# Optimization experiments

Hardware: AMD Instinct MI355X
Metric: run time of the kernel (lower is better)

The kernel has to match this reference:

```python
import jax, jax.numpy as jnp
import numpy as np

N, L, S, C, H = 8, 1024, 1024, 512, 8
SCALE = float((C // H) ** 0.5)  # sqrt(64), as in source (based on embed_dim, not cat'd dim)


def _linear_params(key, c_in, c_out):
    kw, kb = jax.random.split(key)
    lim = 1.0 / np.sqrt(c_in)
    W = jax.random.uniform(kw, (c_out, c_in), jnp.float32, -lim, lim)
    b = jax.random.uniform(kb, (c_out,), jnp.float32, -lim, lim)
    return W, b


def setup_inputs() -> dict:
    key = jax.random.key(0)
    ks = jax.random.split(key, 12)
    inp = {
        'q_c': jax.random.normal(ks[0], (N, L, C), jnp.float32),
        'q_p': jax.random.normal(ks[1], (N, L, C), jnp.float32),
        'k_c': jax.random.normal(ks[2], (N, S, C), jnp.float32),
        'k_p': jax.random.normal(ks[3], (N, S, C), jnp.float32),
        'v': jax.random.normal(ks[4], (N, S, C), jnp.float32),
        'attn_mask': jax.random.normal(ks[5], (N, H, L, S), jnp.float32),
    }
    for i, name in enumerate(['qc', 'qp', 'kc', 'kp', 'v', 'o']):
        W, b = _linear_params(ks[6 + i], C, C)
        inp[f'W_{name}'] = W
        inp[f'b_{name}'] = b
    return inp


def _split_head(x, h):
    n, l, c = x.shape
    return x.reshape(n, l, h, c // h).transpose(0, 2, 1, 3)  # (N,H,L,c/h)


def reference(q_c, q_p, k_c, k_p, v, attn_mask,
              W_qc, b_qc, W_qp, b_qp, W_kc, b_kc, W_kp, b_kp, W_v, b_v, W_o, b_o):
    # dual projections + cat -> (N, L, 2C)
    q = jnp.concatenate([q_c @ W_qc.T + b_qc, q_p @ W_qp.T + b_qp], axis=-1)
    k = jnp.concatenate([k_c @ W_kc.T + b_kc, k_p @ W_kp.T + b_kp], axis=-1)
    vv = v @ W_v.T + b_v
    q = _split_head(q, H)   # (N,H,L,2C/H)
    k = _split_head(k, H)   # (N,H,S,2C/H)
    vv = _split_head(vv, H)  # (N,H,S,C/H)
    attn = jnp.einsum('nhld,nhsd->nhls', q / SCALE, k) + attn_mask
    attn = jax.nn.softmax(attn, axis=-1)
    out = jnp.einsum('nhls,nhsd->nhld', attn, vv)
    out = out.transpose(0, 2, 1, 3).reshape(N, L, C)
    return out @ W_o.T + b_o
```

## Files before the change

### kernel.cpp

```cpp
#include <hip/hip_runtime.h>
#include <hip/hip_bf16.h>

typedef __bf16 bf16;
typedef __bf16 bf16x8 __attribute__((ext_vector_type(8)));
typedef float  f32x4  __attribute__((ext_vector_type(4)));
typedef float  f32x2  __attribute__((ext_vector_type(2)));

#define LOG2E        1.4426950408889634f
#define QSCALE_LOG2E 0.18033688011112043f
#define DEFER_THR    20.0f

#define GLDS(g, l)                                                        \
  __builtin_amdgcn_global_load_lds(                                       \
      (const __attribute__((address_space(1))) void*)(g),                 \
      (__attribute__((address_space(3))) void*)(l), 16, 0, 0)

#define WAITV(n) asm volatile("s_waitcnt vmcnt(" #n ")" ::: "memory")
#define BARRIER() do {                                                    \
  __builtin_amdgcn_s_barrier();                                           \
  __builtin_amdgcn_sched_barrier(0);                                      \
} while (0)

__device__ __forceinline__ void stage_f32_tile(const float* __restrict__ src, int ld,
                                               char* dst, int tid) {
  #pragma unroll
  for (int t = 0; t < 8; ++t) {
    int c8  = tid + t * 256;
    int row = c8 >> 4;
    int h8  = c8 & 15;
    const f32x4 v = *reinterpret_cast<const f32x4*>(src + row * ld + h8 * 4);
    union { bf16 h[4]; unsigned long long u; } pk;
    pk.h[0] = (bf16)v[0]; pk.h[1] = (bf16)v[1];
    pk.h[2] = (bf16)v[2]; pk.h[3] = (bf16)v[3];
    int byte = (row << 7) + ((((h8 >> 1) ^ (row & 7)) << 4) | ((h8 & 1) << 3));
    *reinterpret_cast<unsigned long long*>(dst + byte) = pk.u;
  }
}

__device__ __forceinline__ void stage_bf16_tile(const bf16* __restrict__ src, int ld,
                                                char* dst, int tid) {
  #pragma unroll
  for (int t = 0; t < 4; ++t) {
    int c   = tid + t * 256;
    int row = c >> 3;
    int ck  = c & 7;
    const bf16x8 v = *reinterpret_cast<const bf16x8*>(src + row * ld + ck * 8);
    int byte = (row << 7) + (((ck ^ (row & 7)) << 4));
    *reinterpret_cast<bf16x8*>(dst + byte) = v;
  }
}

__global__ __launch_bounds__(256) void proj_gemm(
    const float* __restrict__ qc, const float* __restrict__ qp,
    const float* __restrict__ kc, const float* __restrict__ kp,
    const float* __restrict__ vin,
    const float* __restrict__ Wqc, const float* __restrict__ bqc,
    const float* __restrict__ Wqp, const float* __restrict__ bqp,
    const float* __restrict__ Wkc, const float* __restrict__ bkc,
    const float* __restrict__ Wkp, const float* __restrict__ bkp,
    const float* __restrict__ Wv,  const float* __restrict__ bv,
    bf16* __restrict__ Qws, bf16* __restrict__ Kws, bf16* __restrict__ Vtws) {
  __shared__ __align__(16) bf16 lA[128 * 64];
  __shared__ __align__(16) bf16 lB[128 * 64];
  char* lAb = (char*)lA;
  char* lBb = (char*)lB;

  const int bxr = blockIdx.x;
  const int bx  = (bxr & 7) * 160 + (bxr >> 3);
  const int g  = bx >> 8;
  const int mt = (bx & 255) >> 2;
  const int nt = bx & 3;

  const float *A, *W, *bias;
  if      (g == 0) { A = qc;  W = Wqc; bias = bqc; }
  else if (g == 1) { A = qp;  W = Wqp; bias = bqp; }
  else if (g == 2) { A = kc;  W = Wkc; bias = bkc; }
  else if (g == 3) { A = kp;  W = Wkp; bias = bkp; }
  else             { A = vin; W = Wv;  bias = bv;  }

  const int tid  = threadIdx.x;
  const int lane = tid & 63, wid = tid >> 6;
  const int wr = wid >> 1, wc = wid & 1;
  const int lrow = lane & 15, lgrp = lane >> 4;

  const float* Abase = A + (size_t)(mt * 128) * 512;
  const float* Wbase = W + (size_t)(nt * 128) * 512;

  const f32x4 fz = {0.f, 0.f, 0.f, 0.f};
  f32x4 acc[4][4];
  #pragma unroll
  for (int i = 0; i < 4; ++i)
    #pragma unroll
    for (int j = 0; j < 4; ++j) acc[i][j] = fz;

  for (int k0 = 0; k0 < 512; k0 += 64) {
    __syncthreads();
    stage_f32_tile(Abase + k0, 512, lAb, tid);
    stage_f32_tile(Wbase + k0, 512, lBb, tid);
    __syncthreads();
    #pragma unroll
    for (int kk = 0; kk < 2; ++kk) {
      bf16x8 af[4], bfr[4];
      #pragma unroll
      for (int mf = 0; mf < 4; ++mf) {
        int row  = wr * 64 + mf * 16 + lrow;
        int byte = (row << 7) + ((((kk << 2) | lgrp) ^ (row & 7)) << 4);
        af[mf] = *reinterpret_cast<const bf16x8*>(lAb + byte);
      }
      #pragma unroll
      for (int nf = 0; nf < 4; ++nf) {
        int row  = wc * 64 + nf * 16 + lrow;
        int byte = (row << 7) + ((((kk << 2) | lgrp) ^ (row & 7)) << 4);
        bfr[nf] = *reinterpret_cast<const bf16x8*>(lBb + byte);
      }
      #pragma unroll
      for (int mf = 0; mf < 4; ++mf)
        #pragma unroll
        for (int nf = 0; nf < 4; ++nf)
          acc[mf][nf] = __builtin_amdgcn_mfma_f32_16x16x32_bf16(
              af[mf], bfr[nf], acc[mf][nf], 0, 0, 0);
    }
  }

  float bcol[4];
  #pragma unroll
  for (int nf = 0; nf < 4; ++nf)
    bcol[nf] = bias[nt * 128 + wc * 64 + nf * 16 + lrow];

  #pragma unroll
  for (int mf = 0; mf < 4; ++mf) {
    #pragma unroll
    for (int nf = 0; nf < 4; ++nf) {
      #pragma unroll
      for (int r = 0; r < 4; ++r) {
        int grow = mt * 128 + wr * 64 + mf * 16 + lgrp * 4 + r;
        int col  = nt * 128 + wc * 64 + nf * 16 + lrow;
        float vv = acc[mf][nf][r] + bcol[nf];
        bf16 hb  = (bf16)vv;
        int n = grow >> 10, tt = grow & 1023;
        if (g < 2) {
          int j = (g << 9) + col;
          Qws[(size_t)((((n << 3) + (j >> 7)) << 10) | tt) * 128 + (j & 127)] = hb;
        } else if (g < 4) {
          int j  = ((g - 2) << 9) + col;
          int hh = j >> 7, d = j & 127;
          int dd = (((d >> 3) ^ ((tt >> 1) & 7)) << 3) | (d & 7);
          Kws[(size_t)((((n << 3) + hh) << 10) | tt) * 128 + dd] = hb;
        } else {
          int h = col >> 6, d = col & 63;
          int kt2 = tt >> 5, si = tt & 31;
          int ss = (((si >> 3) ^ ((d >> 1) & 3)) << 3) | (si & 7);
          Vtws[((size_t)((((n << 3) + h) << 5) + kt2) * 64 + d) * 32 + ss] = hb;
        }
      }
    }
  }
}

__global__ __launch_bounds__(256) void attn_fwd(
    const bf16* __restrict__ Qws, const bf16* __restrict__ Kws,
    const bf16* __restrict__ Vtws, const float* __restrict__ mask,
    bf16* __restrict__ Ows) {
  __shared__ __align__(16) char Kl[3][8192];
  __shared__ __align__(16) char Vl[3][4096];
  __shared__ __align__(16) char Ml[5][8192];
  __shared__ __align__(16) char Pl[4][1024];

  const int bxr = blockIdx.x;
  const int bx  = (bxr & 7) * 128 + (bxr >> 3);
  const int nh = bx >> 4;
  const int qt = bx & 15;
  const int tid = threadIdx.x;
  const int lane = tid & 63, wid = tid >> 6;
  const int lrow = lane & 15, lgrp = lane >> 4;
  const int q0 = qt * 64 + wid * 16;

  const bf16* Qb = Qws + ((size_t)(nh * 1024 + q0 + lrow)) * 128 + lgrp * 8;
  bf16x8 qf[4];
  #pragma unroll
  for (int kk = 0; kk < 4; ++kk)
    qf[kk] = *reinterpret_cast<const bf16x8*>(Qb + kk * 32);

  const float* Mg = mask + ((size_t)(nh * 1024) + qt * 64 + (lane >> 3)) * 1024 +
                    (lane & 7) * 4;
  const bf16* Kg = Kws + (size_t)nh * 131072 + lane * 8;
  const bf16* Vg = Vtws + (size_t)nh * 65536 + lane * 8;

  char* Pb = &Pl[wid][0];

  const f32x4 fz = {0.f, 0.f, 0.f, 0.f};
  f32x4 oacc[4];
  #pragma unroll
  for (int dt = 0; dt < 4; ++dt) oacc[dt] = fz;
  float m2[4], lsum[4];
  #pragma unroll
  for (int r = 0; r < 4; ++r) { m2[r] = 0.f; lsum[r] = 0.f; }

  auto stageM = [&](char* dst, int kt) {
    if (wid == 0) {
      #pragma unroll
      for (int i = 0; i < 8; ++i)
        GLDS(Mg + i * 8192 + kt * 32, dst + i * 1024);
    }
  };
  auto stageKV = [&](char* Kd, char* Vd, int kt) {
    if (wid == 1 || wid == 2) {
      #pragma unroll
      for (int j = 0; j < 4; ++j)
        GLDS(Kg + kt * 4096 + (wid - 1) * 2048 + j * 512,
             Kd + (wid - 1) * 4096 + j * 1024);
    } else if (wid == 3) {
      #pragma unroll
      for (int j = 0; j < 4; ++j)
        GLDS(Vg + kt * 2048 + j * 512, Vd + j * 1024);
    }
  };

  auto compute = [&](const char* Kb, const char* Vb, const char* Mb) {
    bf16x8 kf0[4], kf1[4], vf[4];
    #pragma unroll
    for (int kk = 0; kk < 4; ++kk) {
      int cb = ((((kk << 2) | lgrp) ^ (lrow & 7)) << 4);
      kf0[kk] = *reinterpret_cast<const bf16x8*>(Kb + lrow * 512 + cb);
      kf1[kk] = *reinterpret_cast<const bf16x8*>(Kb + lrow * 512 + 256 + cb);
    }
    #pragma unroll
    for (int dt = 0; dt < 4; ++dt)
      vf[dt] = *reinterpret_cast<const bf16x8*>(
          Vb + (dt * 16 + lrow) * 64 + ((lgrp ^ ((lrow >> 1) & 3)) << 4));
    f32x2 mk[4];
    #pragma unroll
    for (int r = 0; r < 4; ++r) {
      int qrow = wid * 16 + lgrp * 4 + r;
      mk[r] = *reinterpret_cast<const f32x2*>(Mb + qrow * 128 + lrow * 8);
    }

    f32x4 sc0 = fz, sc1 = fz;
    __builtin_amdgcn_s_setprio(1);
    #pragma unroll
    for (int kk = 0; kk < 4; ++kk)
      sc0 = __builtin_amdgcn_mfma_f32_16x16x32_bf16(qf[kk], kf0[kk], sc0, 0, 0, 0);
    #pragma unroll
    for (int kk = 0; kk < 4; ++kk)
      sc1 = __builtin_amdgcn_mfma_f32_16x16x32_bf16(qf[kk], kf1[kk], sc1, 0, 0, 0);
    __builtin_amdgcn_s_setprio(0);

    float a0r[4], a1r[4];
    bool ok = true;
    #pragma unroll
    for (int r = 0; r < 4; ++r) {
      a0r[r] = fmaf(sc0[r], QSCALE_LOG2E, mk[r].x * LOG2E);
      a1r[r] = fmaf(sc1[r], QSCALE_LOG2E, mk[r].y * LOG2E);
      ok &= (fmaxf(a0r[r], a1r[r]) <= m2[r] + DEFER_THR);
    }
    if (__builtin_expect(!__all(ok), 0)) {
      #pragma unroll
      for (int r = 0; r < 4; ++r) {
        float tv = fmaxf(a0r[r], a1r[r]);
        tv = fmaxf(tv, __shfl_xor(tv, 1));
        tv = fmaxf(tv, __shfl_xor(tv, 2));
        tv = fmaxf(tv, __shfl_xor(tv, 4));
        tv = fmaxf(tv, __shfl_xor(tv, 8));
        float mn = fmaxf(m2[r], tv);
        float corr = exp2f(m2[r] - mn);
        m2[r] = mn;
        lsum[r] *= corr;
        #pragma unroll
        for (int dt = 0; dt < 4; ++dt) oacc[dt][r] *= corr;
      }
    }
    #pragma unroll
    for (int r = 0; r < 4; ++r) {
      float e0 = exp2f(a0r[r] - m2[r]);
      float e1 = exp2f(a1r[r] - m2[r]);
      lsum[r] += e0 + e1;
      union { bf16 h[2]; unsigned u; } pk;
      pk.h[0] = (bf16)e0; pk.h[1] = (bf16)e1;
      int row = lgrp * 4 + r;
      int byte = row * 64 + ((((lrow >> 2) ^ (row & 3)) << 4) | ((lrow & 3) << 2));
      *reinterpret_cast<unsigned*>(Pb + byte) = pk.u;
    }
    __builtin_amdgcn_wave_barrier();
    __builtin_amdgcn_sched_barrier(0);
    bf16x8 pf = *reinterpret_cast<const bf16x8*>(
        Pb + lrow * 64 + ((lgrp ^ (lrow & 3)) << 4));

    __builtin_amdgcn_s_setprio(1);
    #pragma unroll
    for (int dt = 0; dt < 4; ++dt)
      oacc[dt] = __builtin_amdgcn_mfma_f32_16x16x32_bf16(pf, vf[dt], oacc[dt], 0, 0, 0);
    __builtin_amdgcn_s_setprio(0);
  };

  char *ka = &Kl[0][0], *kb2 = &Kl[1][0], *kc2 = &Kl[2][0];
  char *va = &Vl[0][0], *vb2 = &Vl[1][0], *vc2 = &Vl[2][0];
  char *m0 = &Ml[0][0], *m1 = &Ml[1][0], *m2p = &Ml[2][0],
       *m3 = &Ml[3][0], *m4 = &Ml[4][0];
  auto rotKV = [&]() {
    char* tp = ka; ka = kb2; kb2 = kc2; kc2 = tp;
    tp = va; va = vb2; vb2 = vc2; vc2 = tp;
  };
  auto rotM = [&]() {
    char* tp = m0; m0 = m1; m1 = m2p; m2p = m3; m3 = m4; m4 = tp;
  };

  stageKV(ka, va, 0);
  stageKV(kb2, vb2, 1);
  stageM(m0, 0); stageM(m1, 1); stageM(m2p, 2); stageM(m3, 3);
  if (wid == 0) { WAITV(24); } else { WAITV(4); }
  BARRIER();

  for (int t = 0; t < 28; ++t) {
    stageKV(kc2, vc2, t + 2);
    stageM(m4, t + 4);
    compute(ka, va, m0);
    if (wid == 0) { WAITV(24); } else { WAITV(4); }
    BARRIER();
    rotKV(); rotM();
  }
  stageKV(kc2, vc2, 30);
  compute(ka, va, m0);
  if (wid == 0) { WAITV(16); } else { WAITV(4); }
  BARRIER(); rotKV(); rotM();

  stageKV(kc2, vc2, 31);
  compute(ka, va, m0);
  if (wid == 0) { WAITV(8); } else { WAITV(4); }
  BARRIER(); rotKV(); rotM();

  compute(ka, va, m0);
  WAITV(0);
  BARRIER(); rotKV(); rotM();

  compute(ka, va, m0);

  #pragma unroll
  for (int r = 0; r < 4; ++r) {
    float ss = lsum[r];
    ss += __shfl_xor(ss, 1);
    ss += __shfl_xor(ss, 2);
    ss += __shfl_xor(ss, 4);
    ss += __shfl_xor(ss, 8);
    lsum[r] = 1.0f / ss;
  }

  const int n = nh >> 3, h = nh & 7;
  bf16* Ob = Ows + ((size_t)(n * 1024 + q0 + lgrp * 4)) * 512 + h * 64 + lrow;
  #pragma unroll
  for (int dt = 0; dt < 4; ++dt)
    #pragma unroll
    for (int r = 0; r < 4; ++r)
      Ob[(size_t)r * 512 + dt * 16] = (bf16)(oacc[dt][r] * lsum[r]);
}

__global__ __launch_bounds__(256) void out_gemm(
    const bf16* __restrict__ Ows, const float* __restrict__ Wo,
    const float* __restrict__ bo, float* __restrict__ out) {
  __shared__ __align__(16) bf16 lA[128 * 64];
  __shared__ __align__(16) bf16 lB[128 * 64];
  char* lAb = (char*)lA;
  char* lBb = (char*)lB;

  const int bxr = blockIdx.x;
  const int bx  = (bxr & 7) * 32 + (bxr >> 3);
  const int mt = bx >> 2;
  const int nt = bx & 3;
  const int tid = threadIdx.x;
  const int lane = tid & 63, wid = tid >> 6;
  const int wr = wid >> 1, wc = wid & 1;
  const int lrow = lane & 15, lgrp = lane >> 4;

  const bf16*  Abase = Ows + (size_t)(mt * 128) * 512;
  const float* Wbase = Wo  + (size_t)(nt * 128) * 512;

  const f32x4 fz = {0.f, 0.f, 0.f, 0.f};
  f32x4 acc[4][4];
  #pragma unroll
  for (int i = 0; i < 4; ++i)
    #pragma unroll
    for (int j = 0; j < 4; ++j) acc[i][j] = fz;

  for (int k0 = 0; k0 < 512; k0 += 64) {
    __syncthreads();
    stage_bf16_tile(Abase + k0, 512, lAb, tid);
    stage_f32_tile(Wbase + k0, 512, lBb, tid);
    __syncthreads();
    #pragma unroll
    for (int kk = 0; kk < 2; ++kk) {
      bf16x8 af[4], bfr[4];
      #pragma unroll
      for (int mf = 0; mf < 4; ++mf) {
        int row  = wr * 64 + mf * 16 + lrow;
        int byte = (row << 7) + ((((kk << 2) | lgrp) ^ (row & 7)) << 4);
        af[mf] = *reinterpret_cast<const bf16x8*>(lAb + byte);
      }
      #pragma unroll
      for (int nf = 0; nf < 4; ++nf) {
        int row  = wc * 64 + nf * 16 + lrow;
        int byte = (row << 7) + ((((kk << 2) | lgrp) ^ (row & 7)) << 4);
        bfr[nf] = *reinterpret_cast<const bf16x8*>(lBb + byte);
      }
      #pragma unroll
      for (int mf = 0; mf < 4; ++mf)
        #pragma unroll
        for (int nf = 0; nf < 4; ++nf)
          acc[mf][nf] = __builtin_amdgcn_mfma_f32_16x16x32_bf16(
              af[mf], bfr[nf], acc[mf][nf], 0, 0, 0);
    }
  }

  float bcol[4];
  #pragma unroll
  for (int nf = 0; nf < 4; ++nf)
    bcol[nf] = bo[nt * 128 + wc * 64 + nf * 16 + lrow];

  #pragma unroll
  for (int mf = 0; mf < 4; ++mf) {
    #pragma unroll
    for (int nf = 0; nf < 4; ++nf) {
      #pragma unroll
      for (int r = 0; r < 4; ++r) {
        int grow = mt * 128 + wr * 64 + mf * 16 + lgrp * 4 + r;
        int col  = nt * 128 + wc * 64 + nf * 16 + lrow;
        out[(size_t)grow * 512 + col] = acc[mf][nf][r] + bcol[nf];
      }
    }
  }
}

extern "C" void kernel_launch(void* const* d_in, const int* in_sizes, int n_in,
                              void* d_out, int out_size, void* d_ws, size_t ws_size,
                              hipStream_t stream) {
  const float* qc   = (const float*)d_in[0];
  const float* qp   = (const float*)d_in[1];
  const float* kc   = (const float*)d_in[2];
  const float* kp   = (const float*)d_in[3];
  const float* vin  = (const float*)d_in[4];
  const float* mask = (const float*)d_in[5];
  const float* Wqc  = (const float*)d_in[6];
  const float* bqc  = (const float*)d_in[7];
  const float* Wqp  = (const float*)d_in[8];
  const float* bqp  = (const float*)d_in[9];
  const float* Wkc  = (const float*)d_in[10];
  const float* bkc  = (const float*)d_in[11];
  const float* Wkp  = (const float*)d_in[12];
  const float* bkp  = (const float*)d_in[13];
  const float* Wv   = (const float*)d_in[14];
  const float* bv   = (const float*)d_in[15];
  const float* Wo   = (const float*)d_in[16];
  const float* bo   = (const float*)d_in[17];

  bf16* Qws  = (bf16*)d_ws;
  bf16* Kws  = Qws  + (size_t)8 * 1024 * 1024;
  bf16* Vtws = Kws  + (size_t)8 * 1024 * 1024;
  bf16* Ows  = Vtws + (size_t)4 * 1024 * 1024;

  proj_gemm<<<dim3(1280), dim3(256), 0, stream>>>(
      qc, qp, kc, kp, vin, Wqc, bqc, Wqp, bqp, Wkc, bkc, Wkp, bkp, Wv, bv,
      Qws, Kws, Vtws);
  attn_fwd<<<dim3(1024), dim3(256), 0, stream>>>(Qws, Kws, Vtws, mask, Ows);
  out_gemm<<<dim3(256), dim3(256), 0, stream>>>(Ows, Wo, bo, (float*)d_out);
}
```

Before: 183.9 us.

## Double KV tile width per iteration and shallow the prefetch pipeline

```diff
diff --git a/kernel.cpp b/kernel.cpp
--- a/kernel.cpp
+++ b/kernel.cpp
@@ -161,10 +161,10 @@
     const bf16* __restrict__ Qws, const bf16* __restrict__ Kws,
     const bf16* __restrict__ Vtws, const float* __restrict__ mask,
     bf16* __restrict__ Ows) {
-  __shared__ __align__(16) char Kl[3][8192];
-  __shared__ __align__(16) char Vl[3][4096];
-  __shared__ __align__(16) char Ml[5][8192];
-  __shared__ __align__(16) char Pl[4][1024];
+  __shared__ __align__(16) char Kl[2][16384];
+  __shared__ __align__(16) char Vl[2][8192];
+  __shared__ __align__(16) char Ml[3][16384];
+  __shared__ __align__(16) char Pl[4][2][1024];
 
   const int bxr = blockIdx.x;
   const int bx  = (bxr & 7) * 128 + (bxr >> 3);
@@ -181,12 +181,13 @@
   for (int kk = 0; kk < 4; ++kk)
     qf[kk] = *reinterpret_cast<const bf16x8*>(Qb + kk * 32);
 
-  const float* Mg = mask + ((size_t)(nh * 1024) + qt * 64 + (lane >> 3)) * 1024 +
-                    (lane & 7) * 4;
+  const float* Mg = mask + ((size_t)(nh * 1024) + qt * 64 + (lane >> 4)) * 1024 +
+                    (lane & 15) * 4;
   const bf16* Kg = Kws + (size_t)nh * 131072 + lane * 8;
   const bf16* Vg = Vtws + (size_t)nh * 65536 + lane * 8;
 
-  char* Pb = &Pl[wid][0];
+  char* PbA = &Pl[wid][0][0];
+  char* PbB = &Pl[wid][1][0];
 
   const f32x4 fz = {0.f, 0.f, 0.f, 0.f};
   f32x4 oacc[4];
@@ -199,64 +200,73 @@
   auto stageM = [&](char* dst, int kt) {
     if (wid == 0) {
       #pragma unroll
-      for (int i = 0; i < 8; ++i)
-        GLDS(Mg + i * 8192 + kt * 32, dst + i * 1024);
+      for (int i = 0; i < 16; ++i)
+        GLDS(Mg + (size_t)i * 4096 + kt * 64, dst + i * 1024);
     }
   };
   auto stageKV = [&](char* Kd, char* Vd, int kt) {
     if (wid == 1 || wid == 2) {
       #pragma unroll
-      for (int j = 0; j < 4; ++j)
-        GLDS(Kg + kt * 4096 + (wid - 1) * 2048 + j * 512,
-             Kd + (wid - 1) * 4096 + j * 1024);
+      for (int j = 0; j < 8; ++j)
+        GLDS(Kg + kt * 8192 + (wid - 1) * 4096 + j * 512,
+             Kd + (wid - 1) * 8192 + j * 1024);
     } else if (wid == 3) {
       #pragma unroll
-      for (int j = 0; j < 4; ++j)
-        GLDS(Vg + kt * 2048 + j * 512, Vd + j * 1024);
+      for (int j = 0; j < 8; ++j)
+        GLDS(Vg + kt * 4096 + j * 512, Vd + j * 1024);
     }
   };
 
   auto compute = [&](const char* Kb, const char* Vb, const char* Mb) {
-    bf16x8 kf0[4], kf1[4], vf[4];
+    bf16x8 ka0[4], ka1[4], kb0[4], kb1[4], vfA[4], vfB[4];
     #pragma unroll
     for (int kk = 0; kk < 4; ++kk) {
       int cb = ((((kk << 2) | lgrp) ^ (lrow & 7)) << 4);
-      kf0[kk] = *reinterpret_cast<const bf16x8*>(Kb + lrow * 512 + cb);
-      kf1[kk] = *reinterpret_cast<const bf16x8*>(Kb + lrow * 512 + 256 + cb);
-    }
-    #pragma unroll
-    for (int dt = 0; dt < 4; ++dt)
-      vf[dt] = *reinterpret_cast<const bf16x8*>(
-          Vb + (dt * 16 + lrow) * 64 + ((lgrp ^ ((lrow >> 1) & 3)) << 4));
-    f32x2 mk[4];
+      ka0[kk] = *reinterpret_cast<const bf16x8*>(Kb + lrow * 512 + cb);
+      ka1[kk] = *reinterpret_cast<const bf16x8*>(Kb + lrow * 512 + 256 + cb);
+      kb0[kk] = *reinterpret_cast<const bf16x8*>(Kb + 8192 + lrow * 512 + cb);
+      kb1[kk] = *reinterpret_cast<const bf16x8*>(Kb + 8192 + lrow * 512 + 256 + cb);
+    }
+    #pragma unroll
+    for (int dt = 0; dt < 4; ++dt) {
+      int vb = (dt * 16 + lrow) * 64 + ((lgrp ^ ((lrow >> 1) & 3)) << 4);
+      vfA[dt] = *reinterpret_cast<const bf16x8*>(Vb + vb);
+      vfB[dt] = *reinterpret_cast<const bf16x8*>(Vb + 4096 + vb);
+    }
+    f32x2 mkA[4], mkB[4];
     #pragma unroll
     for (int r = 0; r < 4; ++r) {
       int qrow = wid * 16 + lgrp * 4 + r;
-      mk[r] = *reinterpret_cast<const f32x2*>(Mb + qrow * 128 + lrow * 8);
-    }
-
-    f32x4 sc0 = fz, sc1 = fz;
+      mkA[r] = *reinterpret_cast<const f32x2*>(Mb + qrow * 256 + lrow * 8);
+      mkB[r] = *reinterpret_cast<const f32x2*>(Mb + qrow * 256 + 128 + lrow * 8);
+    }
+
+    f32x4 sA0 = fz, sA1 = fz, sB0 = fz, sB1 = fz;
     __builtin_amdgcn_s_setprio(1);
     #pragma unroll
-    for (int kk = 0; kk < 4; ++kk)
-      sc0 = __builtin_amdgcn_mfma_f32_16x16x32_bf16(qf[kk], kf0[kk], sc0, 0, 0, 0);
-    #pragma unroll
-    for (int kk = 0; kk < 4; ++kk)
-      sc1 = __builtin_amdgcn_mfma_f32_16x16x32_bf16(qf[kk], kf1[kk], sc1, 0, 0, 0);
+    for (int kk = 0; kk < 4; ++kk) {
+      sA0 = __builtin_amdgcn_mfma_f32_16x16x32_bf16(qf[kk], ka0[kk], sA0, 0, 0, 0);
+      sA1 = __builtin_amdgcn_mfma_f32_16x16x32_bf16(qf[kk], ka1[kk], sA1, 0, 0, 0);
+      sB0 = __builtin_amdgcn_mfma_f32_16x16x32_bf16(qf[kk], kb0[kk], sB0, 0, 0, 0);
+      sB1 = __builtin_amdgcn_mfma_f32_16x16x32_bf16(qf[kk], kb1[kk], sB1, 0, 0, 0);
+    }
     __builtin_amdgcn_s_setprio(0);
 
-    float a0r[4], a1r[4];
+    float aA0[4], aA1[4], aB0[4], aB1[4];
     bool ok = true;
     #pragma unroll
     for (int r = 0; r < 4; ++r) {
-      a0r[r] = fmaf(sc0[r], QSCALE_LOG2E, mk[r].x * LOG2E);
-      a1r[r] = fmaf(sc1[r], QSCALE_LOG2E, mk[r].y * LOG2E);
-      ok &= (fmaxf(a0r[r], a1r[r]) <= m2[r] + DEFER_THR);
+      aA0[r] = fmaf(sA0[r], QSCALE_LOG2E, mkA[r].x * LOG2E);
+      aA1[r] = fmaf(sA1[r], QSCALE_LOG2E, mkA[r].y * LOG2E);
+      aB0[r] = fmaf(sB0[r], QSCALE_LOG2E, mkB[r].x * LOG2E);
+      aB1[r] = fmaf(sB1[r], QSCALE_LOG2E, mkB[r].y * LOG2E);
+      float mx = fmaxf(fmaxf(aA0[r], aA1[r]), fmaxf(aB0[r], aB1[r]));
+      ok &= (mx <= m2[r] + DEFER_THR);
     }
     if (__builtin_expect(!__all(ok), 0)) {
       #pragma unroll
       for (int r = 0; r < 4; ++r) {
-        float tv = fmaxf(a0r[r], a1r[r]);
+        float tv = fmaxf(fmaxf(aA0[r], aA1[r]), fmaxf(aB0[r], aB1[r]));
         tv = fmaxf(tv, __shfl_xor(tv, 1));
         tv = fmaxf(tv, __shfl_xor(tv, 2));
         tv = fmaxf(tv, __shfl_xor(tv, 4));
@@ -271,68 +281,67 @@
     }
     #pragma unroll
     for (int r = 0; r < 4; ++r) {
-      float e0 = exp2f(a0r[r] - m2[r]);
-      float e1 = exp2f(a1r[r] - m2[r]);
-      lsum[r] += e0 + e1;
-      union { bf16 h[2]; unsigned u; } pk;
-      pk.h[0] = (bf16)e0; pk.h[1] = (bf16)e1;
+      float eA0 = exp2f(aA0[r] - m2[r]);
+      float eA1 = exp2f(aA1[r] - m2[r]);
+      float eB0 = exp2f(aB0[r] - m2[r]);
+      float eB1 = exp2f(aB1[r] - m2[r]);
+      lsum[r] += (eA0 + eA1) + (eB0 + eB1);
       int row = lgrp * 4 + r;
       int byte = row * 64 + ((((lrow >> 2) ^ (row & 3)) << 4) | ((lrow & 3) << 2));
-      *reinterpret_cast<unsigned*>(Pb + byte) = pk.u;
+      union { bf16 h[2]; unsigned u; } pa, pb;
+      pa.h[0] = (bf16)eA0; pa.h[1] = (bf16)eA1;
+      pb.h[0] = (bf16)eB0; pb.h[1] = (bf16)eB1;
+      *reinterpret_cast<unsigned*>(PbA + byte) = pa.u;
+      *reinterpret_cast<unsigned*>(PbB + byte) = pb.u;
     }
     __builtin_amdgcn_wave_barrier();
     __builtin_amdgcn_sched_barrier(0);
-    bf16x8 pf = *reinterpret_cast<const bf16x8*>(
-        Pb + lrow * 64 + ((lgrp ^ (lrow & 3)) << 4));
+    int pby = lrow * 64 + ((lgrp ^ (lrow & 3)) << 4);
+    bf16x8 pfA = *reinterpret_cast<const bf16x8*>(PbA + pby);
+    bf16x8 pfB = *reinterpret_cast<const bf16x8*>(PbB + pby);
 
     __builtin_amdgcn_s_setprio(1);
     #pragma unroll
     for (int dt = 0; dt < 4; ++dt)
-      oacc[dt] = __builtin_amdgcn_mfma_f32_16x16x32_bf16(pf, vf[dt], oacc[dt], 0, 0, 0);
+      oacc[dt] = __builtin_amdgcn_mfma_f32_16x16x32_bf16(pfA, vfA[dt], oacc[dt], 0, 0, 0);
+    #pragma unroll
+    for (int dt = 0; dt < 4; ++dt)
+      oacc[dt] = __builtin_amdgcn_mfma_f32_16x16x32_bf16(pfB, vfB[dt], oacc[dt], 0, 0, 0);
     __builtin_amdgcn_s_setprio(0);
   };
 
-  char *ka = &Kl[0][0], *kb2 = &Kl[1][0], *kc2 = &Kl[2][0];
-  char *va = &Vl[0][0], *vb2 = &Vl[1][0], *vc2 = &Vl[2][0];
-  char *m0 = &Ml[0][0], *m1 = &Ml[1][0], *m2p = &Ml[2][0],
-       *m3 = &Ml[3][0], *m4 = &Ml[4][0];
-  auto rotKV = [&]() {
-    char* tp = ka; ka = kb2; kb2 = kc2; kc2 = tp;
-    tp = va; va = vb2; vb2 = vc2; vc2 = tp;
-  };
-  auto rotM = [&]() {
-    char* tp = m0; m0 = m1; m1 = m2p; m2p = m3; m3 = m4; m4 = tp;
-  };
-
-  stageKV(ka, va, 0);
-  stageKV(kb2, vb2, 1);
-  stageM(m0, 0); stageM(m1, 1); stageM(m2p, 2); stageM(m3, 3);
-  if (wid == 0) { WAITV(24); } else { WAITV(4); }
+  char *kcur = &Kl[0][0], *knxt = &Kl[1][0];
+  char *vcur = &Vl[0][0], *vnxt = &Vl[1][0];
+  char *m0 = &Ml[0][0], *m1 = &Ml[1][0], *m2p = &Ml[2][0];
+
+  stageKV(kcur, vcur, 0);
+  stageM(m0, 0);
+  stageM(m1, 1);
+  if (wid == 0) { WAITV(16); } else { WAITV(0); }
   BARRIER();
 
-  for (int t = 0; t < 28; ++t) {
-    stageKV(kc2, vc2, t + 2);
-    stageM(m4, t + 4);
-    compute(ka, va, m0);
-    if (wid == 0) { WAITV(24); } else { WAITV(4); }
+  for (int t = 0; t < 14; ++t) {
+    stageKV(knxt, vnxt, t + 1);
+    stageM(m2p, t + 2);
+    compute(kcur, vcur, m0);
+    if (wid == 0) { WAITV(16); } else { WAITV(0); }
     BARRIER();
-    rotKV(); rotM();
-  }
-  stageKV(kc2, vc2, 30);
-  compute(ka, va, m0);
-  if (wid == 0) { WAITV(16); } else { WAITV(4); }
-  BARRIER(); rotKV(); rotM();
-
-  stageKV(kc2, vc2, 31);
-  compute(ka, va, m0);
-  if (wid == 0) { WAITV(8); } else { WAITV(4); }
-  BARRIER(); rotKV(); rotM();
-
-  compute(ka, va, m0);
+    char* tp;
+    tp = kcur; kcur = knxt; knxt = tp;
+    tp = vcur; vcur = vnxt; vnxt = tp;
+    tp = m0; m0 = m1; m1 = m2p; m2p = tp;
+  }
+  stageKV(knxt, vnxt, 15);
+  compute(kcur, vcur, m0);
   WAITV(0);
-  BARRIER(); rotKV(); rotM();
-
-  compute(ka, va, m0);
+  BARRIER();
+  {
+    char* tp;
+    tp = kcur; kcur = knxt; knxt = tp;
+    tp = vcur; vcur = vnxt; vnxt = tp;
+    tp = m0; m0 = m1; m1 = m2p; m2p = tp;
+  }
+  compute(kcur, vcur, m0);
 
   #pragma unroll
   for (int r = 0; r < 4; ++r) {
```

New measurement: 200.3 us. 8.9% more time.

## Pre-convert projection weights to bf16 and restructure proj GEMM tiling

Applied to the files above, without the earlier changes.

```diff
diff --git a/kernel.cpp b/kernel.cpp
--- a/kernel.cpp
+++ b/kernel.cpp
@@ -21,120 +21,147 @@
   __builtin_amdgcn_sched_barrier(0);                                      \
 } while (0)
 
-__device__ __forceinline__ void stage_f32_tile(const float* __restrict__ src, int ld,
-                                               char* dst, int tid) {
-  #pragma unroll
-  for (int t = 0; t < 8; ++t) {
-    int c8  = tid + t * 256;
-    int row = c8 >> 4;
-    int h8  = c8 & 15;
-    const f32x4 v = *reinterpret_cast<const f32x4*>(src + row * ld + h8 * 4);
-    union { bf16 h[4]; unsigned long long u; } pk;
-    pk.h[0] = (bf16)v[0]; pk.h[1] = (bf16)v[1];
-    pk.h[2] = (bf16)v[2]; pk.h[3] = (bf16)v[3];
-    int byte = (row << 7) + ((((h8 >> 1) ^ (row & 7)) << 4) | ((h8 & 1) << 3));
-    *reinterpret_cast<unsigned long long*>(dst + byte) = pk.u;
-  }
-}
-
-__device__ __forceinline__ void stage_bf16_tile(const bf16* __restrict__ src, int ld,
-                                                char* dst, int tid) {
-  #pragma unroll
-  for (int t = 0; t < 4; ++t) {
-    int c   = tid + t * 256;
-    int row = c >> 3;
-    int ck  = c & 7;
-    const bf16x8 v = *reinterpret_cast<const bf16x8*>(src + row * ld + ck * 8);
-    int byte = (row << 7) + (((ck ^ (row & 7)) << 4));
-    *reinterpret_cast<bf16x8*>(dst + byte) = v;
-  }
+__global__ __launch_bounds__(256) void wconv(
+    const float* __restrict__ Wqc, const float* __restrict__ Wqp,
+    const float* __restrict__ Wkc, const float* __restrict__ Wkp,
+    const float* __restrict__ Wv,  bf16* __restrict__ Wbf) {
+  const int b = blockIdx.x;
+  const int which = b >> 7;
+  const float* src;
+  if      (which == 0) src = Wqc;
+  else if (which == 1) src = Wqp;
+  else if (which == 2) src = Wkc;
+  else if (which == 3) src = Wkp;
+  else                 src = Wv;
+  const int off = (b & 127) * 2048 + threadIdx.x * 8;
+  f32x4 v0 = *reinterpret_cast<const f32x4*>(src + off);
+  f32x4 v1 = *reinterpret_cast<const f32x4*>(src + off + 4);
+  bf16x8 o;
+  o[0] = (bf16)v0[0]; o[1] = (bf16)v0[1]; o[2] = (bf16)v0[2]; o[3] = (bf16)v0[3];
+  o[4] = (bf16)v1[0]; o[5] = (bf16)v1[1]; o[6] = (bf16)v1[2]; o[7] = (bf16)v1[3];
+  *reinterpret_cast<bf16x8*>(Wbf + (size_t)which * 262144 + off) = o;
 }
 
 __global__ __launch_bounds__(256) void proj_gemm(
     const float* __restrict__ qc, const float* __restrict__ qp,
     const float* __restrict__ kc, const float* __restrict__ kp,
     const float* __restrict__ vin,
-    const float* __restrict__ Wqc, const float* __restrict__ bqc,
-    const float* __restrict__ Wqp, const float* __restrict__ bqp,
-    const float* __restrict__ Wkc, const float* __restrict__ bkc,
-    const float* __restrict__ Wkp, const float* __restrict__ bkp,
-    const float* __restrict__ Wv,  const float* __restrict__ bv,
+    const bf16* __restrict__ Wbf,
+    const float* __restrict__ bqc, const float* __restrict__ bqp,
+    const float* __restrict__ bkc, const float* __restrict__ bkp,
+    const float* __restrict__ bv,
     bf16* __restrict__ Qws, bf16* __restrict__ Kws, bf16* __restrict__ Vtws) {
-  __shared__ __align__(16) bf16 lA[128 * 64];
-  __shared__ __align__(16) bf16 lB[128 * 64];
-  char* lAb = (char*)lA;
-  char* lBb = (char*)lB;
+  __shared__ __align__(16) bf16 lA[2][64 * 64];
 
   const int bxr = blockIdx.x;
-  const int bx  = (bxr & 7) * 160 + (bxr >> 3);
-  const int g  = bx >> 8;
-  const int mt = (bx & 255) >> 2;
-  const int nt = bx & 3;
-
-  const float *A, *W, *bias;
-  if      (g == 0) { A = qc;  W = Wqc; bias = bqc; }
-  else if (g == 1) { A = qp;  W = Wqp; bias = bqp; }
-  else if (g == 2) { A = kc;  W = Wkc; bias = bkc; }
-  else if (g == 3) { A = kp;  W = Wkp; bias = bkp; }
-  else             { A = vin; W = Wv;  bias = bv;  }
+  const int bx  = (bxr & 7) * 80 + (bxr >> 3);
+  const int g   = bx >> 7;
+  const int mt  = bx & 127;
+
+  const float *A, *bias;
+  if      (g == 0) { A = qc;  bias = bqc; }
+  else if (g == 1) { A = qp;  bias = bqp; }
+  else if (g == 2) { A = kc;  bias = bkc; }
+  else if (g == 3) { A = kp;  bias = bkp; }
+  else             { A = vin; bias = bv;  }
+  const bf16* Wg = Wbf + (size_t)g * 262144;
 
   const int tid  = threadIdx.x;
   const int lane = tid & 63, wid = tid >> 6;
-  const int wr = wid >> 1, wc = wid & 1;
   const int lrow = lane & 15, lgrp = lane >> 4;
 
-  const float* Abase = A + (size_t)(mt * 128) * 512;
-  const float* Wbase = W + (size_t)(nt * 128) * 512;
+  const float* Abase = A + (size_t)(mt * 64) * 512;
+
+  int srow[4], sh8[4];
+  #pragma unroll
+  for (int t = 0; t < 4; ++t) {
+    int c8 = tid + t * 256;
+    srow[t] = c8 >> 4;
+    sh8[t]  = c8 & 15;
+  }
+
+  const bf16* wrow[8];
+  #pragma unroll
+  for (int nf = 0; nf < 8; ++nf)
+    wrow[nf] = Wg + (size_t)(wid * 128 + nf * 16 + lrow) * 512 + lgrp * 8;
 
   const f32x4 fz = {0.f, 0.f, 0.f, 0.f};
-  f32x4 acc[4][4];
+  f32x4 acc[4][8];
   #pragma unroll
   for (int i = 0; i < 4; ++i)
     #pragma unroll
-    for (int j = 0; j < 4; ++j) acc[i][j] = fz;
-
-  for (int k0 = 0; k0 < 512; k0 += 64) {
-    __syncthreads();
-    stage_f32_tile(Abase + k0, 512, lAb, tid);
-    stage_f32_tile(Wbase + k0, 512, lBb, tid);
-    __syncthreads();
+    for (int j = 0; j < 8; ++j) acc[i][j] = fz;
+
+  auto stage_write = [&](f32x4 (&v)[4], int buf) {
+    char* dst = (char*)&lA[buf][0];
+    #pragma unroll
+    for (int t = 0; t < 4; ++t) {
+      union { bf16 h[4]; unsigned long long u; } pk;
+      pk.h[0] = (bf16)v[t][0]; pk.h[1] = (bf16)v[t][1];
+      pk.h[2] = (bf16)v[t][2]; pk.h[3] = (bf16)v[t][3];
+      int byte = (srow[t] << 7) +
+                 ((((sh8[t] >> 1) ^ (srow[t] & 7)) << 4) | ((sh8[t] & 1) << 3));
+      *reinterpret_cast<unsigned long long*>(dst + byte) = pk.u;
+    }
+  };
+
+  {
+    f32x4 v[4];
+    #pragma unroll
+    for (int t = 0; t < 4; ++t)
+      v[t] = *reinterpret_cast<const f32x4*>(Abase + srow[t] * 512 + sh8[t] * 4);
+    stage_write(v, 0);
+  }
+  __syncthreads();
+
+  for (int t = 0; t < 8; ++t) {
+    const int k0 = t * 64;
+    f32x4 aR[4];
+    if (t < 7) {
+      #pragma unroll
+      for (int u = 0; u < 4; ++u)
+        aR[u] = *reinterpret_cast<const f32x4*>(
+            Abase + srow[u] * 512 + sh8[u] * 4 + k0 + 64);
+    }
+    const char* lAb = (const char*)&lA[t & 1][0];
     #pragma unroll
     for (int kk = 0; kk < 2; ++kk) {
-      bf16x8 af[4], bfr[4];
+      bf16x8 af[4], wf[8];
       #pragma unroll
       for (int mf = 0; mf < 4; ++mf) {
-        int row  = wr * 64 + mf * 16 + lrow;
+        int row  = mf * 16 + lrow;
         int byte = (row << 7) + ((((kk << 2) | lgrp) ^ (row & 7)) << 4);
         af[mf] = *reinterpret_cast<const bf16x8*>(lAb + byte);
       }
       #pragma unroll
-      for (int nf = 0; nf < 4; ++nf) {
-        int row  = wc * 64 + nf * 16 + lrow;
-        int byte = (row << 7) + ((((kk << 2) | lgrp) ^ (row & 7)) << 4);
-        bfr[nf] = *reinterpret_cast<const bf16x8*>(lBb + byte);
-      }
+      for (int nf = 0; nf < 8; ++nf)
+        wf[nf] = *reinterpret_cast<const bf16x8*>(wrow[nf] + k0 + kk * 32);
       #pragma unroll
       for (int mf = 0; mf < 4; ++mf)
         #pragma unroll
-        for (int nf = 0; nf < 4; ++nf)
+        for (int nf = 0; nf < 8; ++nf)
           acc[mf][nf] = __builtin_amdgcn_mfma_f32_16x16x32_bf16(
-              af[mf], bfr[nf], acc[mf][nf], 0, 0, 0);
-    }
-  }
-
-  float bcol[4];
-  #pragma unroll
-  for (int nf = 0; nf < 4; ++nf)
-    bcol[nf] = bias[nt * 128 + wc * 64 + nf * 16 + lrow];
+              af[mf], wf[nf], acc[mf][nf], 0, 0, 0);
+    }
+    if (t < 7) {
+      stage_write(aR, (t + 1) & 1);
+      __syncthreads();
+    }
+  }
+
+  float bcol[8];
+  #pragma unroll
+  for (int nf = 0; nf < 8; ++nf)
+    bcol[nf] = bias[wid * 128 + nf * 16 + lrow];
 
   #pragma unroll
   for (int mf = 0; mf < 4; ++mf) {
     #pragma unroll
-    for (int nf = 0; nf < 4; ++nf) {
+    for (int nf = 0; nf < 8; ++nf) {
       #pragma unroll
       for (int r = 0; r < 4; ++r) {
-        int grow = mt * 128 + wr * 64 + mf * 16 + lgrp * 4 + r;
-        int col  = nt * 128 + wc * 64 + nf * 16 + lrow;
+        int grow = mt * 64 + mf * 16 + lgrp * 4 + r;
+        int col  = wid * 128 + nf * 16 + lrow;
         float vv = acc[mf][nf][r] + bcol[nf];
         bf16 hb  = (bf16)vv;
         int n = grow >> 10, tt = grow & 1023;
@@ -351,6 +378,35 @@
     #pragma unroll
     for (int r = 0; r < 4; ++r)
       Ob[(size_t)r * 512 + dt * 16] = (bf16)(oacc[dt][r] * lsum[r]);
+}
+
+__device__ __forceinline__ void stage_f32_tile(const float* __restrict__ src, int ld,
+                                               char* dst, int tid) {
+  #pragma unroll
+  for (int t = 0; t < 8; ++t) {
+    int c8  = tid + t * 256;
+    int row = c8 >> 4;
+    int h8  = c8 & 15;
+    const f32x4 v = *reinterpret_cast<const f32x4*>(src + row * ld + h8 * 4);
+    union { bf16 h[4]; unsigned long long u; } pk;
+    pk.h[0] = (bf16)v[0]; pk.h[1] = (bf16)v[1];
+    pk.h[2] = (bf16)v[2]; pk.h[3] = (bf16)v[3];
+    int byte = (row << 7) + ((((h8 >> 1) ^ (row & 7)) << 4) | ((h8 & 1) << 3));
+    *reinterpret_cast<unsigned long long*>(dst + byte) = pk.u;
+  }
+}
+
+__device__ __forceinline__ void stage_bf16_tile(const bf16* __restrict__ src, int ld,
+                                                char* dst, int tid) {
+  #pragma unroll
+  for (int t = 0; t < 4; ++t) {
+    int c   = tid + t * 256;
+    int row = c >> 3;
+    int ck  = c & 7;
+    const bf16x8 v = *reinterpret_cast<const bf16x8*>(src + row * ld + ck * 8);
+    int byte = (row << 7) + (((ck ^ (row & 7)) << 4));
+    *reinterpret_cast<bf16x8*>(dst + byte) = v;
+  }
 }
 
 __global__ __launch_bounds__(256) void out_gemm(
@@ -454,10 +510,11 @@
   bf16* Kws  = Qws  + (size_t)8 * 1024 * 1024;
   bf16* Vtws = Kws  + (size_t)8 * 1024 * 1024;
   bf16* Ows  = Vtws + (size_t)4 * 1024 * 1024;
-
-  proj_gemm<<<dim3(1280), dim3(256), 0, stream>>>(
-      qc, qp, kc, kp, vin, Wqc, bqc, Wqp, bqp, Wkc, bkc, Wkp, bkp, Wv, bv,
-      Qws, Kws, Vtws);
+  bf16* Wbf  = Ows  + (size_t)4 * 1024 * 1024;
+
+  wconv<<<dim3(640), dim3(256), 0, stream>>>(Wqc, Wqp, Wkc, Wkp, Wv, Wbf);
+  proj_gemm<<<dim3(640), dim3(256), 0, stream>>>(
+      qc, qp, kc, kp, vin, Wbf, bqc, bqp, bkc, bkp, bv, Qws, Kws, Vtws);
   attn_fwd<<<dim3(1024), dim3(256), 0, stream>>>(Qws, Kws, Vtws, mask, Ows);
   out_gemm<<<dim3(256), dim3(256), 0, stream>>>(Ows, Wo, bo, (float*)d_out);
 }
```

After: 224.7 us. 22.2% more time.
